# Optimization experiments

Measured on AMD Instinct MI355X. Metric: run time of the kernel, lower is better.

Reference implementation:

```python
import jax, jax.numpy as jnp
import numpy as np

B, H, W = 1, 32, 32
C, G, K = 128, 4, 15
GC = C // G          # group channels = 32
K2 = K * K           # 225
RED = 4              # SE reduction
KHID = 32            # kernel_net hidden


def setup_inputs() -> dict:
    key = jax.random.key(0)
    ks = jax.random.split(key, 24)
    def n(k, shape, s=0.02):
        return jax.random.normal(k, shape, jnp.float32) * s
    inp = {
        'x': jax.random.normal(ks[0], (B, H, W, C), jnp.float32),
        # scalars (torch: raw_sigma init = softplus^{-1}(0.3), base_offset_scale = 0.1)
        'raw_sigma': jnp.asarray(float(np.log(np.expm1(0.3))), jnp.float32),
        'base_offset_scale': jnp.asarray(0.1, jnp.float32),
        # input/output projections
        'w_in': n(ks[1], (C, C)), 'b_in': jnp.zeros((C,), jnp.float32),
        'w_out': n(ks[2], (C, C)), 'b_out': jnp.zeros((C,), jnp.float32),
        # dw_conv: depthwise 3x3 (HWIO, I=1 per group) + pointwise 1x1
        'dw_k': n(ks[3], (3, 3, 1, C), 0.1), 'dw_b': jnp.zeros((C,), jnp.float32),
        'pw_w': n(ks[4], (C, C)), 'pw_b': jnp.zeros((C,), jnp.float32),
        # offset / mask nets (zero-init in torch; small random here to exercise gather)
        'off_w': n(ks[5], (C, G * K2 * 2), 0.01), 'off_b': n(ks[6], (G * K2 * 2,), 0.01),
        'msk_w': n(ks[7], (C, G * K2), 0.01), 'msk_b': n(ks[8], (G * K2,), 0.01),
        # kernel_net: 2 -> 32 -> 32 -> G*GC
        'k1_w': n(ks[9], (2, KHID), 0.3), 'k1_b': jnp.zeros((KHID,), jnp.float32),
        'k2_w': n(ks[10], (KHID, KHID), 0.2), 'k2_b': jnp.zeros((KHID,), jnp.float32),
        'k3_w': n(ks[11], (KHID, G * GC), 0.2), 'k3_b': jnp.zeros((G * GC,), jnp.float32),
        # SE block
        'se1_w': n(ks[12], (C, C // RED), 0.1), 'se1_b': jnp.zeros((C // RED,), jnp.float32),
        'se2_w': n(ks[13], (C // RED, C), 0.1), 'se2_b': jnp.zeros((C,), jnp.float32),
    }
    return inp


def reference(x, raw_sigma, base_offset_scale, w_in, b_in, w_out, b_out,
              dw_k, dw_b, pw_w, pw_b, off_w, off_b, msk_w, msk_b,
              k1_w, k1_b, k2_w, k2_b, k3_w, k3_b, se1_w, se1_b, se2_w, se2_b):
    # sigma (scalar path, biases=None)
    sigma = jnp.clip(jax.nn.softplus(raw_sigma), 0.001, 0.5)
    grid = jnp.linspace(-0.5, 0.5, K)

    x_proj = x @ w_in + b_in                                   # [B,H,W,C]

    # dw_conv: depthwise 3x3 -> SiLU -> 1x1
    y = jax.lax.conv_general_dilated(
        x, dw_k, (1, 1), 'SAME',
        dimension_numbers=('NHWC', 'HWIO', 'NHWC'),
        feature_group_count=C) + dw_b
    x_dw = jax.nn.silu(y) @ pw_w + pw_b                        # [B,H,W,C]

    # Gaussian envelope over kernel grid, normalized (scalar sigma -> shape [K,K])
    gh = grid[:, None]; gw = grid[None, :]
    env = jnp.exp(-(gh ** 2 + gw ** 2) / (2.0 * sigma ** 2))
    env = env / jnp.clip(env.sum(), 1e-8)                      # [K,K]

    # dynamic kernel weights from grid positions (*2); replicate torch's
    # contiguous view (K,K,G,gc) -> (G,K2,gc)
    pos = jnp.stack(jnp.meshgrid(grid, grid, indexing='ij'), -1).reshape(K2, 2) * 2.0
    h1 = jax.nn.silu(pos @ k1_w + k1_b)
    h2 = jax.nn.silu(h1 @ k2_w + k2_b)
    kw = (h2 @ k3_w + k3_b).reshape(K, K, G, GC).reshape(G, K2, GC)  # [G,K2,gc]

    offsets = (x_dw @ off_w + off_b).reshape(B, H, W, G, K2, 2) * base_offset_scale
    raw_mask = (x_dw @ msk_w + msk_b).reshape(B, H, W, G, K2) * env.reshape(1, 1, 1, 1, K2)
    attn = jnp.nan_to_num(jax.nn.softmax(raw_mask, axis=-1))   # [B,H,W,G,K2]

    # reference sampling grid (integer offsets -K//2..K//2)
    ref = jnp.linspace(-(K // 2), K // 2, K)
    ref_grid = jnp.stack(jnp.meshgrid(ref, ref, indexing='ij'), -1).reshape(K2, 2)
    pos_h = jnp.arange(H, dtype=jnp.float32).reshape(1, H, 1, 1, 1)
    pos_w = jnp.arange(W, dtype=jnp.float32).reshape(1, 1, W, 1, 1)

    abs_h = pos_h + ref_grid[:, 0].reshape(1, 1, 1, 1, K2) + offsets[..., 0]
    abs_w = pos_w + ref_grid[:, 1].reshape(1, 1, 1, 1, K2) + offsets[..., 1]
    ah = jnp.clip(abs_h, 0.0, H - 1); aw = jnp.clip(abs_w, 0.0, W - 1)
    hf = jnp.clip(ah.astype(jnp.int32), 0, H - 1)
    wf = jnp.clip(aw.astype(jnp.int32), 0, W - 1)
    hc = jnp.clip(hf + 1, 0, H - 1)
    wc = jnp.clip(wf + 1, 0, W - 1)
    hw = ah - hf.astype(jnp.float32)
    ww = aw - wf.astype(jnp.float32)
    valid = (~((abs_h < 0) | (abs_h > H - 1) | (abs_w < 0) | (abs_w > W - 1))).astype(jnp.float32)

    x_g = x_proj.reshape(B, H, W, G, GC)
    b_idx = jnp.arange(B).reshape(B, 1, 1, 1, 1)
    g_idx = jnp.arange(G).reshape(1, 1, 1, G, 1)
    def gather(hi, wi):
        return x_g[b_idx, hi, wi, g_idx]                       # [B,H,W,G,K2,gc]

    sampled = (gather(hf, wf) * ((1 - hw) * (1 - ww) * valid)[..., None]
             + gather(hf, wc) * ((1 - hw) * ww * valid)[..., None]
             + gather(hc, wf) * (hw * (1 - ww) * valid)[..., None]
             + gather(hc, wc) * (hw * ww * valid)[..., None])

    sampled = sampled * kw.reshape(1, 1, 1, G, K2, GC)
    out = jnp.einsum('bhwgkc,bhwgk->bhwgc', sampled, attn).reshape(B, H, W, C)

    # SE block (mask=None, bias=None)
    pooled = out.mean(axis=(1, 2), keepdims=True)
    scale = jax.nn.sigmoid(jax.nn.silu(pooled @ se1_w + se1_b) @ se2_w + se2_b)
    out = out * scale

    return out @ w_out + b_out
```

## Files before the change

### kernel.cpp

```cpp
#include <hip/hip_runtime.h>
#include <math.h>

constexpr int H = 32, W = 32, C = 128, G = 4, K = 15, K2 = 225, GC = 32;
constexpr int NPIX = H * W;
constexpr int NOFF = G * K2 * 2;
constexpr int NMSK = G * K2;
constexpr int NTOT = NOFF + NMSK;
constexpr int KHID = 32;

constexpr size_t WS_ENV    = 0;
constexpr size_t WS_KW     = 256;
constexpr size_t WS_SCALE  = 29184;
constexpr size_t WS_PART   = 29312;
constexpr size_t WS_XPROJ  = 33792;
constexpr size_t WS_XDW    = 164864;
constexpr size_t WS_OUTPRE = 295936;
constexpr size_t WS_OFFS   = 427008;
constexpr size_t WS_MASK   = 2270208;

__device__ __forceinline__ float sigmoidf_(float v) { return 1.f / (1.f + expf(-v)); }
__device__ __forceinline__ float siluf_(float v)    { return v / (1.f + expf(-v)); }

__device__ __forceinline__ void mlp_point(int k2i, int lane,
                                          const float* __restrict__ k1_w, const float* __restrict__ k1_b,
                                          const float* __restrict__ k2_w, const float* __restrict__ k2_b,
                                          const float* __restrict__ k3_w, const float* __restrict__ k3_b,
                                          float* __restrict__ ws) {
    int i = k2i / 15, j = k2i % 15;
    float ph = (-0.5f + (float)i * (1.f / 14.f)) * 2.f;
    float pw = (-0.5f + (float)j * (1.f / 14.f)) * 2.f;
    float h1[KHID], h2[KHID];
#pragma unroll
    for (int m = 0; m < KHID; m++)
        h1[m] = siluf_(fmaf(ph, k1_w[m], fmaf(pw, k1_w[KHID + m], k1_b[m])));
#pragma unroll
    for (int m = 0; m < KHID; m++) {
        float a = k2_b[m];
#pragma unroll
        for (int q = 0; q < KHID; q++) a = fmaf(h1[q], k2_w[q * KHID + m], a);
        h2[m] = siluf_(a);
    }
#pragma unroll
    for (int t = 0; t < 2; t++) {
        int col = lane + t * 64;
        float a = k3_b[col];
#pragma unroll
        for (int q = 0; q < KHID; q++) a = fmaf(h2[q], k3_w[q * C + col], a);
        ws[WS_KW + (size_t)k2i * C + col] = a;
    }
}

__global__ __launch_bounds__(256) void prep_kernel(const float* __restrict__ raw_sigma,
                             const float* __restrict__ k1_w, const float* __restrict__ k1_b,
                             const float* __restrict__ k2_w, const float* __restrict__ k2_b,
                             const float* __restrict__ k3_w, const float* __restrict__ k3_b,
                             float* __restrict__ ws) {
    int tid = threadIdx.x;
    if (blockIdx.x == 0) {
        __shared__ float red[256];
        float xs = raw_sigma[0];
        float sp = fmaxf(xs, 0.f) + log1pf(expf(-fabsf(xs)));
        float sigma = fminf(fmaxf(sp, 0.001f), 0.5f);
        float inv2s2 = 1.f / (2.f * sigma * sigma);
        int i = tid / 15, j = tid % 15;
        float e = 0.f;
        if (tid < K2) {
            float gi = -0.5f + (float)i * (1.f / 14.f);
            float gj = -0.5f + (float)j * (1.f / 14.f);
            e = expf(-(gi * gi + gj * gj) * inv2s2);
        }
        red[tid] = e;
        __syncthreads();
        for (int s = 128; s > 0; s >>= 1) {
            if (tid < s) red[tid] += red[tid + s];
            __syncthreads();
        }
        float esum = fmaxf(red[0], 1e-8f);
        if (tid < K2) ws[WS_ENV + tid] = e / esum;
        if (tid < 64) mlp_point(224, tid, k1_w, k1_b, k2_w, k2_b, k3_w, k3_b, ws);
    } else {
        int k2i = (blockIdx.x - 1) * 4 + (tid >> 6);
        mlp_point(k2i, tid & 63, k1_w, k1_b, k2_w, k2_b, k3_w, k3_b, ws);
    }
}

__global__ __launch_bounds__(256) void front_kernel(const float* __restrict__ x,
                             const float* __restrict__ w_in, const float* __restrict__ b_in,
                             const float* __restrict__ dw_k, const float* __restrict__ dw_b,
                             const float* __restrict__ pw_w, const float* __restrict__ pw_b,
                             float* __restrict__ ws) {
    int p0 = blockIdx.x * 4;
    int tid = threadIdx.x;
    int c = tid & 127;
    int pp = tid >> 7;
    __shared__ float xs[4][C], ts[4][C];
#pragma unroll
    for (int q = 0; q < 2; q++) {
        int px = pp * 2 + q;
        int p = p0 + px;
        int h = p >> 5, w = p & 31;
        xs[px][c] = x[(size_t)p * C + c];
        float y = dw_b[c];
#pragma unroll
        for (int dy = 0; dy < 3; dy++) {
            int hh = h + dy - 1;
            if (hh < 0 || hh >= H) continue;
#pragma unroll
            for (int dx = 0; dx < 3; dx++) {
                int wq = w + dx - 1;
                if (wq < 0 || wq >= W) continue;
                y = fmaf(x[((size_t)hh * W + wq) * C + c], dw_k[(dy * 3 + dx) * C + c], y);
            }
        }
        ts[px][c] = siluf_(y);
    }
    __syncthreads();
    float ap0 = b_in[c], ap1 = b_in[c], ad0 = pw_b[c], ad1 = pw_b[c];
    int b0 = pp * 2, b1 = pp * 2 + 1;
    for (int i = 0; i < C; i += 4) {
#pragma unroll
        for (int u = 0; u < 4; u++) {
            float wi = w_in[(size_t)(i + u) * C + c];
            float pi = pw_w[(size_t)(i + u) * C + c];
            ap0 = fmaf(xs[b0][i + u], wi, ap0);
            ap1 = fmaf(xs[b1][i + u], wi, ap1);
            ad0 = fmaf(ts[b0][i + u], pi, ad0);
            ad1 = fmaf(ts[b1][i + u], pi, ad1);
        }
    }
    ws[WS_XPROJ + (size_t)(p0 + b0) * C + c] = ap0;
    ws[WS_XPROJ + (size_t)(p0 + b1) * C + c] = ap1;
    ws[WS_XDW  + (size_t)(p0 + b0) * C + c] = ad0;
    ws[WS_XDW  + (size_t)(p0 + b1) * C + c] = ad1;
}

__global__ __launch_bounds__(256) void offmsk_gemm(const float* __restrict__ A,
                                                   const float* __restrict__ off_w,
                                                   const float* __restrict__ off_b,
                                                   const float* __restrict__ msk_w,
                                                   const float* __restrict__ msk_b,
                                                   const float* __restrict__ bos,
                                                   const float* __restrict__ env,
                                                   float* __restrict__ offs_out,
                                                   float* __restrict__ mask_out) {
    __shared__ float At[32][72];
    __shared__ float Bs[32][64];
    int tid = threadIdx.x;
    int c0 = blockIdx.x * 64;
    int p0 = blockIdx.y * 64;
    int tx = tid & 15, ty = tid >> 4;

    float acc[4][4];
#pragma unroll
    for (int i = 0; i < 4; i++)
#pragma unroll
        for (int j = 0; j < 4; j++) acc[i][j] = 0.f;

    int cL = (tid * 4) & 63;
    int kL = (tid * 4) >> 6;
    int cB = c0 + cL;
    const float* bptr = nullptr; int bstride = 0;
    if (cB < NOFF)       { bptr = off_w + cB;          bstride = NOFF; }
    else if (cB < NTOT)  { bptr = msk_w + (cB - NOFF); bstride = NMSK; }
    int rA = tid >> 3, k4A = (tid & 7) * 4;

    for (int kt = 0; kt < C; kt += 32) {
        if (kt) __syncthreads();
#pragma unroll
        for (int pass = 0; pass < 2; pass++) {
            int r = rA + pass * 32;
            float4 v = *(const float4*)&A[(size_t)(p0 + r) * C + kt + k4A];
            At[k4A + 0][r] = v.x; At[k4A + 1][r] = v.y;
            At[k4A + 2][r] = v.z; At[k4A + 3][r] = v.w;
            int k = kL + pass * 16;
            float4 bv = make_float4(0.f, 0.f, 0.f, 0.f);
            if (bptr) bv = *(const float4*)&bptr[(size_t)(kt + k) * bstride];
            *(float4*)&Bs[k][cL] = bv;
        }
        __syncthreads();
#pragma unroll
        for (int k = 0; k < 32; k++) {
            float4 a4 = *(const float4*)&At[k][ty * 4];
            float4 b4 = *(const float4*)&Bs[k][tx * 4];
            const float av[4] = {a4.x, a4.y, a4.z, a4.w};
            const float bv[4] = {b4.x, b4.y, b4.z, b4.w};
#pragma unroll
            for (int i = 0; i < 4; i++)
#pragma unroll
                for (int j = 0; j < 4; j++)
                    acc[i][j] = fmaf(av[i], bv[j], acc[i][j]);
        }
    }

    int colbase = c0 + tx * 4;
    if (colbase >= NTOT) return;
    float bias[4], sc[4];
    float* obase;
    int ostride;
    if (colbase < NOFF) {
        float s = bos[0];
#pragma unroll
        for (int j = 0; j < 4; j++) { bias[j] = off_b[colbase + j]; sc[j] = s; }
        obase = offs_out + colbase; ostride = NOFF;
    } else {
        int m0 = colbase - NOFF;
#pragma unroll
        for (int j = 0; j < 4; j++) { bias[j] = msk_b[m0 + j]; sc[j] = env[(m0 + j) % K2]; }
        obase = mask_out + m0; ostride = NMSK;
    }
#pragma unroll
    for (int i = 0; i < 4; i++) {
        size_t row = (size_t)(p0 + ty * 4 + i);
        float4 r0 = make_float4((acc[i][0] + bias[0]) * sc[0], (acc[i][1] + bias[1]) * sc[1],
                                (acc[i][2] + bias[2]) * sc[2], (acc[i][3] + bias[3]) * sc[3]);
        *(float4*)&obase[row * ostride] = r0;
    }
}

__global__ __launch_bounds__(256) void sampler_kernel(const float* __restrict__ ws_offs,
                                                      const float* __restrict__ ws_mask,
                                                      const float* __restrict__ xproj,
                                                      const float* __restrict__ kwf,
                                                      float* __restrict__ outpre) {
    int p0 = blockIdx.x * 2;
    int h = p0 >> 5;
    int tid = threadIdx.x;

    __shared__ float   attn_s[2][NMSK];
    __shared__ float4  wgt_s[2][NMSK];
    __shared__ ushort4 loc_s[2][NMSK];

    {
        int half = tid >> 5;
        int l32 = tid & 31;
        int px = half >> 2, g = half & 3;
        const float* mrow = ws_mask + (size_t)(p0 + px) * NMSK + g * K2;
        float v[8];
        float mx = -1e30f;
#pragma unroll
        for (int q = 0; q < 8; q++) {
            int k = l32 + q * 32;
            v[q] = (k < K2) ? mrow[k] : -1e30f;
            mx = fmaxf(mx, v[q]);
        }
#pragma unroll
        for (int s = 16; s > 0; s >>= 1) mx = fmaxf(mx, __shfl_xor(mx, s));
        float sum = 0.f;
#pragma unroll
        for (int q = 0; q < 8; q++) {
            int k = l32 + q * 32;
            v[q] = (k < K2) ? expf(v[q] - mx) : 0.f;
            sum += v[q];
        }
#pragma unroll
        for (int s = 16; s > 0; s >>= 1) sum += __shfl_xor(sum, s);
        float inv = 1.f / sum;
#pragma unroll
        for (int q = 0; q < 8; q++) {
            int k = l32 + q * 32;
            if (k < K2) attn_s[px][g * K2 + k] = v[q] * inv;
        }
    }
    __syncthreads();

    for (int e = tid; e < 2 * NMSK; e += 256) {
        int px = (e >= NMSK) ? 1 : 0;
        int m = e - px * NMSK;
        int g = m / K2;
        int k = m - g * K2;
        int p = p0 + px;
        int w = p & 31;
        float2 o = *(const float2*)&ws_offs[(size_t)p * NOFF + m * 2];
        float abs_h = (float)(h + k / 15 - 7) + o.x;
        float abs_w = (float)(w + k % 15 - 7) + o.y;
        float validf = (abs_h < 0.f || abs_h > 31.f || abs_w < 0.f || abs_w > 31.f) ? 0.f : 1.f;
        float ah = fminf(fmaxf(abs_h, 0.f), 31.f);
        float aw = fminf(fmaxf(abs_w, 0.f), 31.f);
        int hf = (int)ah, wf = (int)aw;
        int hc = min(hf + 1, 31), wc = min(wf + 1, 31);
        float hwt = ah - (float)hf, wwt = aw - (float)wf;
        float a = attn_s[px][m] * validf;
        float u0 = 1.f - hwt, u1 = 1.f - wwt;
        wgt_s[px][m] = make_float4(a * u0 * u1, a * u0 * wwt, a * hwt * u1, a * hwt * wwt);
        loc_s[px][m] = make_ushort4((unsigned short)(hf * W + wf), (unsigned short)(hf * W + wc),
                                    (unsigned short)(hc * W + wf), (unsigned short)(hc * W + wc));
    }
    __syncthreads();

    {
        int cq = tid & 7;
        int s  = (tid >> 3) & 3;
        int g  = (tid >> 5) & 3;
        int px = tid >> 7;
        int k0 = (s * K2) >> 2;
        int k1 = ((s + 1) * K2) >> 2;
        const float* xpg = xproj + g * GC + cq * 4;
        const float* kwg = kwf + (size_t)g * (K2 * GC) + cq * 4;
        float4 acc = make_float4(0.f, 0.f, 0.f, 0.f);
        for (int k = k0; k < k1; k++) {
            int m = g * K2 + k;
            ushort4 L  = loc_s[px][m];
            float4  Wv = wgt_s[px][m];
            float4 x00 = *(const float4*)(xpg + (int)L.x * C);
            float4 x01 = *(const float4*)(xpg + (int)L.y * C);
            float4 x10 = *(const float4*)(xpg + (int)L.z * C);
            float4 x11 = *(const float4*)(xpg + (int)L.w * C);
            float4 kw4 = *(const float4*)(kwg + k * GC);
            float sx = fmaf(Wv.w, x11.x, fmaf(Wv.z, x10.x, fmaf(Wv.y, x01.x, Wv.x * x00.x)));
            float sy = fmaf(Wv.w, x11.y, fmaf(Wv.z, x10.y, fmaf(Wv.y, x01.y, Wv.x * x00.y)));
            float sz = fmaf(Wv.w, x11.z, fmaf(Wv.z, x10.z, fmaf(Wv.y, x01.z, Wv.x * x00.z)));
            float sw = fmaf(Wv.w, x11.w, fmaf(Wv.z, x10.w, fmaf(Wv.y, x01.w, Wv.x * x00.w)));
            acc.x = fmaf(kw4.x, sx, acc.x);
            acc.y = fmaf(kw4.y, sy, acc.y);
            acc.z = fmaf(kw4.z, sz, acc.z);
            acc.w = fmaf(kw4.w, sw, acc.w);
        }
        acc.x += __shfl_xor(acc.x, 8);  acc.y += __shfl_xor(acc.y, 8);
        acc.z += __shfl_xor(acc.z, 8);  acc.w += __shfl_xor(acc.w, 8);
        acc.x += __shfl_xor(acc.x, 16); acc.y += __shfl_xor(acc.y, 16);
        acc.z += __shfl_xor(acc.z, 16); acc.w += __shfl_xor(acc.w, 16);
        if (s == 0)
            *(float4*)&outpre[(size_t)(p0 + px) * C + g * GC + cq * 4] = acc;
    }
}

__global__ void reduce1_kernel(const float* __restrict__ outpre, float* __restrict__ part) {
    int b = blockIdx.x;
    int c = threadIdx.x;
    float s = 0.f;
    for (int q = 0; q < 32; q++) s += outpre[(size_t)(b * 32 + q) * C + c];
    part[(size_t)b * C + c] = s;
}

__global__ void se_kernel(const float* __restrict__ part,
                          const float* __restrict__ se1_w, const float* __restrict__ se1_b,
                          const float* __restrict__ se2_w, const float* __restrict__ se2_b,
                          float* __restrict__ scale_out) {
    __shared__ float pooled[C];
    __shared__ float hid[KHID];
    int tid = threadIdx.x;
    float s = 0.f;
    for (int b = 0; b < 32; b++) s += part[(size_t)b * C + tid];
    pooled[tid] = s * (1.f / 1024.f);
    __syncthreads();
    if (tid < KHID) {
        float a = se1_b[tid];
        for (int cc = 0; cc < C; cc++) a = fmaf(pooled[cc], se1_w[cc * KHID + tid], a);
        hid[tid] = siluf_(a);
    }
    __syncthreads();
    float a = se2_b[tid];
#pragma unroll
    for (int q = 0; q < KHID; q++) a = fmaf(hid[q], se2_w[q * C + tid], a);
    scale_out[tid] = sigmoidf_(a);
}

__global__ __launch_bounds__(256) void final_kernel(const float* __restrict__ outpre,
                             const float* __restrict__ scale,
                             const float* __restrict__ w_out, const float* __restrict__ b_out,
                             float* __restrict__ out) {
    int p0 = blockIdx.x * 4;
    int tid = threadIdx.x;
    int c = tid & 127;
    int pp = tid >> 7;
    __shared__ float v[4][C];
    float scv = scale[c];
#pragma unroll
    for (int q = 0; q < 2; q++) {
        int px = pp * 2 + q;
        v[px][c] = outpre[(size_t)(p0 + px) * C + c] * scv;
    }
    __syncthreads();
    float a0 = b_out[c], a1 = b_out[c];
    int b0 = pp * 2, b1 = pp * 2 + 1;
    for (int i = 0; i < C; i += 4) {
#pragma unroll
        for (int u = 0; u < 4; u++) {
            float wv = w_out[(size_t)(i + u) * C + c];
            a0 = fmaf(v[b0][i + u], wv, a0);
            a1 = fmaf(v[b1][i + u], wv, a1);
        }
    }
    out[(size_t)(p0 + b0) * C + c] = a0;
    out[(size_t)(p0 + b1) * C + c] = a1;
}

extern "C" void kernel_launch(void* const* d_in, const int* in_sizes, int n_in,
                              void* d_out, int out_size, void* d_ws, size_t ws_size,
                              hipStream_t stream) {
    const float* x         = (const float*)d_in[0];
    const float* raw_sigma = (const float*)d_in[1];
    const float* bos       = (const float*)d_in[2];
    const float* w_in      = (const float*)d_in[3];
    const float* b_in      = (const float*)d_in[4];
    const float* w_out     = (const float*)d_in[5];
    const float* b_out     = (const float*)d_in[6];
    const float* dw_k      = (const float*)d_in[7];
    const float* dw_b      = (const float*)d_in[8];
    const float* pw_w      = (const float*)d_in[9];
    const float* pw_b      = (const float*)d_in[10];
    const float* off_w     = (const float*)d_in[11];
    const float* off_b     = (const float*)d_in[12];
    const float* msk_w     = (const float*)d_in[13];
    const float* msk_b     = (const float*)d_in[14];
    const float* k1_w      = (const float*)d_in[15];
    const float* k1_b      = (const float*)d_in[16];
    const float* k2_w      = (const float*)d_in[17];
    const float* k2_b      = (const float*)d_in[18];
    const float* k3_w      = (const float*)d_in[19];
    const float* k3_b      = (const float*)d_in[20];
    const float* se1_w     = (const float*)d_in[21];
    const float* se1_b     = (const float*)d_in[22];
    const float* se2_w     = (const float*)d_in[23];
    const float* se2_b     = (const float*)d_in[24];

    float* ws  = (float*)d_ws;
    float* out = (float*)d_out;

    prep_kernel<<<57, 256, 0, stream>>>(raw_sigma, k1_w, k1_b, k2_w, k2_b, k3_w, k3_b, ws);
    front_kernel<<<NPIX / 4, 256, 0, stream>>>(x, w_in, b_in, dw_k, dw_b, pw_w, pw_b, ws);

    dim3 gg((NTOT + 63) / 64, NPIX / 64);
    offmsk_gemm<<<gg, 256, 0, stream>>>(ws + WS_XDW, off_w, off_b, msk_w, msk_b, bos,
                                        ws + WS_ENV, ws + WS_OFFS, ws + WS_MASK);

    sampler_kernel<<<NPIX / 2, 256, 0, stream>>>(ws + WS_OFFS, ws + WS_MASK, ws + WS_XPROJ,
                                                 ws + WS_KW, ws + WS_OUTPRE);

    reduce1_kernel<<<32, C, 0, stream>>>(ws + WS_OUTPRE, ws + WS_PART);
    se_kernel<<<1, C, 0, stream>>>(ws + WS_PART, se1_w, se1_b, se2_w, se2_b, ws + WS_SCALE);
    final_kernel<<<NPIX / 4, 256, 0, stream>>>(ws + WS_OUTPRE, ws + WS_SCALE, w_out, b_out, out);
}
```

Measured before the change: 81.26 us.

## Fuse prep/front and SE/final kernels, enlarge offset GEMM tiles

Merges the prep and front kernels into one launch and moves the SE pooling partial sums into the sampler epilogue. Every block of a new finale kernel redundantly computes the SE scale before applying the output projection, which cuts the launch count from seven to four and removes the separate reduce and SE passes. The offset/mask GEMM moves from 64x64 tiles with 4x4 per-thread outputs to 128x128 tiles with 8x8, plus tail guards on partial columns. The changes trade launch overhead for redundant SE work in all 256 finale blocks, and the larger GEMM tiles mean fewer blocks and higher register pressure.

```diff
diff --git a/kernel.cpp b/kernel.cpp
--- a/kernel.cpp
+++ b/kernel.cpp
@@ -8,24 +8,23 @@
 constexpr int NTOT = NOFF + NMSK;
 constexpr int KHID = 32;
 
-constexpr size_t WS_ENV    = 0;
-constexpr size_t WS_KW     = 256;
-constexpr size_t WS_SCALE  = 29184;
-constexpr size_t WS_PART   = 29312;
-constexpr size_t WS_XPROJ  = 33792;
-constexpr size_t WS_XDW    = 164864;
-constexpr size_t WS_OUTPRE = 295936;
-constexpr size_t WS_OFFS   = 427008;
-constexpr size_t WS_MASK   = 2270208;
+constexpr size_t WS_ENV    = 128;
+constexpr size_t WS_KW     = 384;
+constexpr size_t WS_PART   = 29184;
+constexpr size_t WS_XPROJ  = 94720;
+constexpr size_t WS_XDW    = 225792;
+constexpr size_t WS_OFFS   = 356864;
+constexpr size_t WS_MASK   = 2200064;
+constexpr size_t WS_OUTPRE = 3121664;
 
 __device__ __forceinline__ float sigmoidf_(float v) { return 1.f / (1.f + expf(-v)); }
 __device__ __forceinline__ float siluf_(float v)    { return v / (1.f + expf(-v)); }
 
 __device__ __forceinline__ void mlp_point(int k2i, int lane,
-                                          const float* __restrict__ k1_w, const float* __restrict__ k1_b,
-                                          const float* __restrict__ k2_w, const float* __restrict__ k2_b,
-                                          const float* __restrict__ k3_w, const float* __restrict__ k3_b,
-                                          float* __restrict__ ws) {
+        const float* __restrict__ k1_w, const float* __restrict__ k1_b,
+        const float* __restrict__ k2_w, const float* __restrict__ k2_b,
+        const float* __restrict__ k3_w, const float* __restrict__ k3_b,
+        float* __restrict__ ws) {
     int i = k2i / 15, j = k2i % 15;
     float ph = (-0.5f + (float)i * (1.f / 14.f)) * 2.f;
     float pw = (-0.5f + (float)j * (1.f / 14.f)) * 2.f;
@@ -50,114 +49,110 @@
     }
 }
 
-__global__ __launch_bounds__(256) void prep_kernel(const float* __restrict__ raw_sigma,
-                             const float* __restrict__ k1_w, const float* __restrict__ k1_b,
-                             const float* __restrict__ k2_w, const float* __restrict__ k2_b,
-                             const float* __restrict__ k3_w, const float* __restrict__ k3_b,
-                             float* __restrict__ ws) {
+__global__ __launch_bounds__(256) void prep_front_kernel(const float* __restrict__ x,
+        const float* __restrict__ raw_sigma,
+        const float* __restrict__ w_in, const float* __restrict__ b_in,
+        const float* __restrict__ dw_k, const float* __restrict__ dw_b,
+        const float* __restrict__ pw_w, const float* __restrict__ pw_b,
+        const float* __restrict__ k1_w, const float* __restrict__ k1_b,
+        const float* __restrict__ k2_w, const float* __restrict__ k2_b,
+        const float* __restrict__ k3_w, const float* __restrict__ k3_b,
+        float* __restrict__ ws) {
     int tid = threadIdx.x;
-    if (blockIdx.x == 0) {
-        __shared__ float red[256];
-        float xs = raw_sigma[0];
-        float sp = fmaxf(xs, 0.f) + log1pf(expf(-fabsf(xs)));
-        float sigma = fminf(fmaxf(sp, 0.001f), 0.5f);
-        float inv2s2 = 1.f / (2.f * sigma * sigma);
-        int i = tid / 15, j = tid % 15;
-        float e = 0.f;
-        if (tid < K2) {
-            float gi = -0.5f + (float)i * (1.f / 14.f);
-            float gj = -0.5f + (float)j * (1.f / 14.f);
-            e = expf(-(gi * gi + gj * gj) * inv2s2);
-        }
-        red[tid] = e;
+    int b = blockIdx.x;
+    if (b < 256) {
+        __shared__ float xs[4][C], ts[4][C];
+        int p0 = b * 4;
+        int c = tid & 127, pp = tid >> 7;
+#pragma unroll
+        for (int q = 0; q < 2; q++) {
+            int px = pp * 2 + q;
+            int p = p0 + px;
+            int h = p >> 5, w = p & 31;
+            xs[px][c] = x[(size_t)p * C + c];
+            float y = dw_b[c];
+#pragma unroll
+            for (int dy = 0; dy < 3; dy++) {
+                int hh = h + dy - 1;
+                if (hh < 0 || hh >= H) continue;
+#pragma unroll
+                for (int dx = 0; dx < 3; dx++) {
+                    int wq = w + dx - 1;
+                    if (wq < 0 || wq >= W) continue;
+                    y = fmaf(x[((size_t)hh * W + wq) * C + c], dw_k[(dy * 3 + dx) * C + c], y);
+                }
+            }
+            ts[px][c] = siluf_(y);
+        }
         __syncthreads();
-        for (int s = 128; s > 0; s >>= 1) {
-            if (tid < s) red[tid] += red[tid + s];
+        float ap0 = b_in[c], ap1 = ap0, ad0 = pw_b[c], ad1 = ad0;
+        int b0 = pp * 2, b1 = pp * 2 + 1;
+        for (int i = 0; i < C; i += 4) {
+#pragma unroll
+            for (int u = 0; u < 4; u++) {
+                float wi = w_in[(size_t)(i + u) * C + c];
+                float pi = pw_w[(size_t)(i + u) * C + c];
+                ap0 = fmaf(xs[b0][i + u], wi, ap0);
+                ap1 = fmaf(xs[b1][i + u], wi, ap1);
+                ad0 = fmaf(ts[b0][i + u], pi, ad0);
+                ad1 = fmaf(ts[b1][i + u], pi, ad1);
+            }
+        }
+        ws[WS_XPROJ + (size_t)(p0 + b0) * C + c] = ap0;
+        ws[WS_XPROJ + (size_t)(p0 + b1) * C + c] = ap1;
+        ws[WS_XDW  + (size_t)(p0 + b0) * C + c] = ad0;
+        ws[WS_XDW  + (size_t)(p0 + b1) * C + c] = ad1;
+    } else {
+        int mb = b - 256;
+        if (mb == 0) {
+            __shared__ float red[256];
+            float xsg = raw_sigma[0];
+            float sp = fmaxf(xsg, 0.f) + log1pf(expf(-fabsf(xsg)));
+            float sigma = fminf(fmaxf(sp, 0.001f), 0.5f);
+            float inv2s2 = 1.f / (2.f * sigma * sigma);
+            int i = tid / 15, j = tid % 15;
+            float e = 0.f;
+            if (tid < K2) {
+                float gi = -0.5f + (float)i * (1.f / 14.f);
+                float gj = -0.5f + (float)j * (1.f / 14.f);
+                e = expf(-(gi * gi + gj * gj) * inv2s2);
+            }
+            red[tid] = e;
             __syncthreads();
-        }
-        float esum = fmaxf(red[0], 1e-8f);
-        if (tid < K2) ws[WS_ENV + tid] = e / esum;
-        if (tid < 64) mlp_point(224, tid, k1_w, k1_b, k2_w, k2_b, k3_w, k3_b, ws);
-    } else {
-        int k2i = (blockIdx.x - 1) * 4 + (tid >> 6);
-        mlp_point(k2i, tid & 63, k1_w, k1_b, k2_w, k2_b, k3_w, k3_b, ws);
-    }
-}
-
-__global__ __launch_bounds__(256) void front_kernel(const float* __restrict__ x,
-                             const float* __restrict__ w_in, const float* __restrict__ b_in,
-                             const float* __restrict__ dw_k, const float* __restrict__ dw_b,
-                             const float* __restrict__ pw_w, const float* __restrict__ pw_b,
-                             float* __restrict__ ws) {
-    int p0 = blockIdx.x * 4;
+            for (int s = 128; s > 0; s >>= 1) {
+                if (tid < s) red[tid] += red[tid + s];
+                __syncthreads();
+            }
+            float esum = fmaxf(red[0], 1e-8f);
+            if (tid < K2) ws[WS_ENV + tid] = e / esum;
+            if (tid < 64) mlp_point(224, tid, k1_w, k1_b, k2_w, k2_b, k3_w, k3_b, ws);
+        } else {
+            int k2i = (mb - 1) * 4 + (tid >> 6);
+            mlp_point(k2i, tid & 63, k1_w, k1_b, k2_w, k2_b, k3_w, k3_b, ws);
+        }
+    }
+}
+
+__global__ __launch_bounds__(256) void offmsk_gemm(const float* __restrict__ A,
+        const float* __restrict__ off_w, const float* __restrict__ off_b,
+        const float* __restrict__ msk_w, const float* __restrict__ msk_b,
+        const float* __restrict__ bos, const float* __restrict__ env,
+        float* __restrict__ offs_out, float* __restrict__ mask_out) {
+    __shared__ float At[32][132];
+    __shared__ float Bs[32][128];
     int tid = threadIdx.x;
-    int c = tid & 127;
-    int pp = tid >> 7;
-    __shared__ float xs[4][C], ts[4][C];
-#pragma unroll
-    for (int q = 0; q < 2; q++) {
-        int px = pp * 2 + q;
-        int p = p0 + px;
-        int h = p >> 5, w = p & 31;
-        xs[px][c] = x[(size_t)p * C + c];
-        float y = dw_b[c];
-#pragma unroll
-        for (int dy = 0; dy < 3; dy++) {
-            int hh = h + dy - 1;
-            if (hh < 0 || hh >= H) continue;
-#pragma unroll
-            for (int dx = 0; dx < 3; dx++) {
-                int wq = w + dx - 1;
-                if (wq < 0 || wq >= W) continue;
-                y = fmaf(x[((size_t)hh * W + wq) * C + c], dw_k[(dy * 3 + dx) * C + c], y);
-            }
-        }
-        ts[px][c] = siluf_(y);
-    }
-    __syncthreads();
-    float ap0 = b_in[c], ap1 = b_in[c], ad0 = pw_b[c], ad1 = pw_b[c];
-    int b0 = pp * 2, b1 = pp * 2 + 1;
-    for (int i = 0; i < C; i += 4) {
-#pragma unroll
-        for (int u = 0; u < 4; u++) {
-            float wi = w_in[(size_t)(i + u) * C + c];
-            float pi = pw_w[(size_t)(i + u) * C + c];
-            ap0 = fmaf(xs[b0][i + u], wi, ap0);
-            ap1 = fmaf(xs[b1][i + u], wi, ap1);
-            ad0 = fmaf(ts[b0][i + u], pi, ad0);
-            ad1 = fmaf(ts[b1][i + u], pi, ad1);
-        }
-    }
-    ws[WS_XPROJ + (size_t)(p0 + b0) * C + c] = ap0;
-    ws[WS_XPROJ + (size_t)(p0 + b1) * C + c] = ap1;
-    ws[WS_XDW  + (size_t)(p0 + b0) * C + c] = ad0;
-    ws[WS_XDW  + (size_t)(p0 + b1) * C + c] = ad1;
-}
-
-__global__ __launch_bounds__(256) void offmsk_gemm(const float* __restrict__ A,
-                                                   const float* __restrict__ off_w,
-                                                   const float* __restrict__ off_b,
-                                                   const float* __restrict__ msk_w,
-                                                   const float* __restrict__ msk_b,
-                                                   const float* __restrict__ bos,
-                                                   const float* __restrict__ env,
-                                                   float* __restrict__ offs_out,
-                                                   float* __restrict__ mask_out) {
-    __shared__ float At[32][72];
-    __shared__ float Bs[32][64];
-    int tid = threadIdx.x;
-    int c0 = blockIdx.x * 64;
-    int p0 = blockIdx.y * 64;
+    int c0 = blockIdx.x * 128;
+    int p0 = blockIdx.y * 128;
     int tx = tid & 15, ty = tid >> 4;
 
-    float acc[4][4];
-#pragma unroll
-    for (int i = 0; i < 4; i++)
-#pragma unroll
-        for (int j = 0; j < 4; j++) acc[i][j] = 0.f;
-
-    int cL = (tid * 4) & 63;
-    int kL = (tid * 4) >> 6;
+    float acc[8][8];
+#pragma unroll
+    for (int i = 0; i < 8; i++)
+#pragma unroll
+        for (int j = 0; j < 8; j++) acc[i][j] = 0.f;
+
+    int cL = (tid & 31) * 4;
+    int kB = tid >> 5;
     int cB = c0 + cL;
     const float* bptr = nullptr; int bstride = 0;
     if (cB < NOFF)       { bptr = off_w + cB;          bstride = NOFF; }
@@ -167,68 +162,88 @@
     for (int kt = 0; kt < C; kt += 32) {
         if (kt) __syncthreads();
 #pragma unroll
-        for (int pass = 0; pass < 2; pass++) {
+        for (int pass = 0; pass < 4; pass++) {
             int r = rA + pass * 32;
             float4 v = *(const float4*)&A[(size_t)(p0 + r) * C + kt + k4A];
             At[k4A + 0][r] = v.x; At[k4A + 1][r] = v.y;
             At[k4A + 2][r] = v.z; At[k4A + 3][r] = v.w;
-            int k = kL + pass * 16;
+        }
+#pragma unroll
+        for (int pass = 0; pass < 4; pass++) {
+            int k = kB + pass * 8;
             float4 bv = make_float4(0.f, 0.f, 0.f, 0.f);
             if (bptr) bv = *(const float4*)&bptr[(size_t)(kt + k) * bstride];
             *(float4*)&Bs[k][cL] = bv;
         }
         __syncthreads();
-#pragma unroll
+#pragma unroll 4
         for (int k = 0; k < 32; k++) {
-            float4 a4 = *(const float4*)&At[k][ty * 4];
-            float4 b4 = *(const float4*)&Bs[k][tx * 4];
-            const float av[4] = {a4.x, a4.y, a4.z, a4.w};
-            const float bv[4] = {b4.x, b4.y, b4.z, b4.w};
-#pragma unroll
-            for (int i = 0; i < 4; i++)
-#pragma unroll
-                for (int j = 0; j < 4; j++)
+            float4 a0 = *(const float4*)&At[k][ty * 8];
+            float4 a1 = *(const float4*)&At[k][ty * 8 + 4];
+            float4 b0 = *(const float4*)&Bs[k][tx * 8];
+            float4 b1 = *(const float4*)&Bs[k][tx * 8 + 4];
+            const float av[8] = {a0.x, a0.y, a0.z, a0.w, a1.x, a1.y, a1.z, a1.w};
+            const float bv[8] = {b0.x, b0.y, b0.z, b0.w, b1.x, b1.y, b1.z, b1.w};
+#pragma unroll
+            for (int i = 0; i < 8; i++)
+#pragma unroll
+                for (int j = 0; j < 8; j++)
                     acc[i][j] = fmaf(av[i], bv[j], acc[i][j]);
         }
     }
 
-    int colbase = c0 + tx * 4;
+    int colbase = c0 + tx * 8;
     if (colbase >= NTOT) return;
-    float bias[4], sc[4];
+    bool full = (colbase + 8) <= NTOT;
+    float bias[8], sc[8];
     float* obase;
     int ostride;
     if (colbase < NOFF) {
         float s = bos[0];
 #pragma unroll
-        for (int j = 0; j < 4; j++) { bias[j] = off_b[colbase + j]; sc[j] = s; }
+        for (int j = 0; j < 8; j++) { bias[j] = off_b[colbase + j]; sc[j] = s; }
         obase = offs_out + colbase; ostride = NOFF;
     } else {
         int m0 = colbase - NOFF;
 #pragma unroll
-        for (int j = 0; j < 4; j++) { bias[j] = msk_b[m0 + j]; sc[j] = env[(m0 + j) % K2]; }
+        for (int j = 0; j < 8; j++) {
+            if (colbase + j < NTOT) { bias[j] = msk_b[m0 + j]; sc[j] = env[(m0 + j) % K2]; }
+            else                    { bias[j] = 0.f; sc[j] = 0.f; }
+        }
         obase = mask_out + m0; ostride = NMSK;
     }
 #pragma unroll
-    for (int i = 0; i < 4; i++) {
-        size_t row = (size_t)(p0 + ty * 4 + i);
-        float4 r0 = make_float4((acc[i][0] + bias[0]) * sc[0], (acc[i][1] + bias[1]) * sc[1],
-                                (acc[i][2] + bias[2]) * sc[2], (acc[i][3] + bias[3]) * sc[3]);
-        *(float4*)&obase[row * ostride] = r0;
+    for (int i = 0; i < 8; i++) {
+        size_t row = (size_t)(p0 + ty * 8 + i);
+        if (full) {
+            float4 r0 = make_float4((acc[i][0] + bias[0]) * sc[0], (acc[i][1] + bias[1]) * sc[1],
+                                    (acc[i][2] + bias[2]) * sc[2], (acc[i][3] + bias[3]) * sc[3]);
+            float4 r1 = make_float4((acc[i][4] + bias[4]) * sc[4], (acc[i][5] + bias[5]) * sc[5],
+                                    (acc[i][6] + bias[6]) * sc[6], (acc[i][7] + bias[7]) * sc[7]);
+            *(float4*)&obase[row * ostride]     = r0;
+            *(float4*)&obase[row * ostride + 4] = r1;
+        } else {
+#pragma unroll
+            for (int j = 0; j < 8; j++)
+                if (colbase + j < NTOT)
+                    obase[row * ostride + j] = (acc[i][j] + bias[j]) * sc[j];
+        }
     }
 }
 
 __global__ __launch_bounds__(256) void sampler_kernel(const float* __restrict__ ws_offs,
-                                                      const float* __restrict__ ws_mask,
-                                                      const float* __restrict__ xproj,
-                                                      const float* __restrict__ kwf,
-                                                      float* __restrict__ outpre) {
-    int p0 = blockIdx.x * 2;
+        const float* __restrict__ ws_mask, const float* __restrict__ xproj,
+        const float* __restrict__ kwf, float* __restrict__ outpre,
+        float* __restrict__ partial) {
+    int blk = blockIdx.x;
+    int p0 = blk * 2;
     int h = p0 >> 5;
     int tid = threadIdx.x;
 
     __shared__ float   attn_s[2][NMSK];
     __shared__ float4  wgt_s[2][NMSK];
     __shared__ ushort4 loc_s[2][NMSK];
+    __shared__ float   outp[2][C];
 
     {
         int half = tid >> 5;
@@ -297,6 +312,7 @@
         const float* xpg = xproj + g * GC + cq * 4;
         const float* kwg = kwf + (size_t)g * (K2 * GC) + cq * 4;
         float4 acc = make_float4(0.f, 0.f, 0.f, 0.f);
+#pragma unroll 2
         for (int k = k0; k < k1; k++) {
             int m = g * K2 + k;
             ushort4 L  = loc_s[px][m];
@@ -319,29 +335,45 @@
         acc.z += __shfl_xor(acc.z, 8);  acc.w += __shfl_xor(acc.w, 8);
         acc.x += __shfl_xor(acc.x, 16); acc.y += __shfl_xor(acc.y, 16);
         acc.z += __shfl_xor(acc.z, 16); acc.w += __shfl_xor(acc.w, 16);
-        if (s == 0)
+        if (s == 0) {
+            *(float4*)&outp[px][g * GC + cq * 4] = acc;
             *(float4*)&outpre[(size_t)(p0 + px) * C + g * GC + cq * 4] = acc;
-    }
-}
-
-__global__ void reduce1_kernel(const float* __restrict__ outpre, float* __restrict__ part) {
-    int b = blockIdx.x;
-    int c = threadIdx.x;
-    float s = 0.f;
-    for (int q = 0; q < 32; q++) s += outpre[(size_t)(b * 32 + q) * C + c];
-    part[(size_t)b * C + c] = s;
-}
-
-__global__ void se_kernel(const float* __restrict__ part,
-                          const float* __restrict__ se1_w, const float* __restrict__ se1_b,
-                          const float* __restrict__ se2_w, const float* __restrict__ se2_b,
-                          float* __restrict__ scale_out) {
+        }
+    }
+    __syncthreads();
+    if (tid < C)
+        partial[(size_t)blk * C + tid] = outp[0][tid] + outp[1][tid];
+}
+
+__global__ __launch_bounds__(256) void finale_kernel(const float* __restrict__ outpre,
+        const float* __restrict__ partial,
+        const float* __restrict__ se1_w, const float* __restrict__ se1_b,
+        const float* __restrict__ se2_w, const float* __restrict__ se2_b,
+        const float* __restrict__ w_out, const float* __restrict__ b_out,
+        float* __restrict__ out) {
+    int tid = threadIdx.x;
+    __shared__ float tmp[8][132];
     __shared__ float pooled[C];
     __shared__ float hid[KHID];
-    int tid = threadIdx.x;
-    float s = 0.f;
-    for (int b = 0; b < 32; b++) s += part[(size_t)b * C + tid];
-    pooled[tid] = s * (1.f / 1024.f);
+    __shared__ float scl[C];
+    __shared__ float v[4][C];
+
+    {
+        int bg = tid >> 5, c4 = (tid & 31) * 4;
+        float4 s4 = make_float4(0.f, 0.f, 0.f, 0.f);
+        for (int i = 0; i < 64; i++) {
+            float4 pv = *(const float4*)&partial[(size_t)(bg * 64 + i) * C + c4];
+            s4.x += pv.x; s4.y += pv.y; s4.z += pv.z; s4.w += pv.w;
+        }
+        *(float4*)&tmp[bg][c4] = s4;
+    }
+    __syncthreads();
+    if (tid < C) {
+        float s = 0.f;
+#pragma unroll
+        for (int g = 0; g < 8; g++) s += tmp[g][tid];
+        pooled[tid] = s * (1.f / 1024.f);
+    }
     __syncthreads();
     if (tid < KHID) {
         float a = se1_b[tid];
@@ -349,26 +381,20 @@
         hid[tid] = siluf_(a);
     }
     __syncthreads();
-    float a = se2_b[tid];
-#pragma unroll
-    for (int q = 0; q < KHID; q++) a = fmaf(hid[q], se2_w[q * C + tid], a);
-    scale_out[tid] = sigmoidf_(a);
-}
-
-__global__ __launch_bounds__(256) void final_kernel(const float* __restrict__ outpre,
-                             const float* __restrict__ scale,
-                             const float* __restrict__ w_out, const float* __restrict__ b_out,
-                             float* __restrict__ out) {
+    if (tid < C) {
+        float a = se2_b[tid];
+#pragma unroll
+        for (int q = 0; q < KHID; q++) a = fmaf(hid[q], se2_w[q * C + tid], a);
+        scl[tid] = sigmoidf_(a);
+    }
+    __syncthreads();
+
     int p0 = blockIdx.x * 4;
-    int tid = threadIdx.x;
-    int c = tid & 127;
-    int pp = tid >> 7;
-    __shared__ float v[4][C];
-    float scv = scale[c];
+    int c = tid & 127, pp = tid >> 7;
 #pragma unroll
     for (int q = 0; q < 2; q++) {
         int px = pp * 2 + q;
-        v[px][c] = outpre[(size_t)(p0 + px) * C + c] * scv;
+        v[px][c] = outpre[(size_t)(p0 + px) * C + c] * scl[c];
     }
     __syncthreads();
     float a0 = b_out[c], a1 = b_out[c];
@@ -417,17 +443,18 @@
     float* ws  = (float*)d_ws;
     float* out = (float*)d_out;
 
-    prep_kernel<<<57, 256, 0, stream>>>(raw_sigma, k1_w, k1_b, k2_w, k2_b, k3_w, k3_b, ws);
-    front_kernel<<<NPIX / 4, 256, 0, stream>>>(x, w_in, b_in, dw_k, dw_b, pw_w, pw_b, ws);
-
-    dim3 gg((NTOT + 63) / 64, NPIX / 64);
+    prep_front_kernel<<<313, 256, 0, stream>>>(x, raw_sigma, w_in, b_in, dw_k, dw_b,
+                                               pw_w, pw_b, k1_w, k1_b, k2_w, k2_b,
+                                               k3_w, k3_b, ws);
+
+    dim3 gg((NTOT + 127) / 128, NPIX / 128);
     offmsk_gemm<<<gg, 256, 0, stream>>>(ws + WS_XDW, off_w, off_b, msk_w, msk_b, bos,
                                         ws + WS_ENV, ws + WS_OFFS, ws + WS_MASK);
 
     sampler_kernel<<<NPIX / 2, 256, 0, stream>>>(ws + WS_OFFS, ws + WS_MASK, ws + WS_XPROJ,
-                                                 ws + WS_KW, ws + WS_OUTPRE);
-
-    reduce1_kernel<<<32, C, 0, stream>>>(ws + WS_OUTPRE, ws + WS_PART);
-    se_kernel<<<1, C, 0, stream>>>(ws + WS_PART, se1_w, se1_b, se2_w, se2_b, ws + WS_SCALE);
-    final_kernel<<<NPIX / 4, 256, 0, stream>>>(ws + WS_OUTPRE, ws + WS_SCALE, w_out, b_out, out);
-}
+                                                 ws + WS_KW, ws + WS_OUTPRE, ws + WS_PART);
+
+    finale_kernel<<<NPIX / 4, 256, 0, stream>>>(ws + WS_OUTPRE, ws + WS_PART,
+                                                se1_w, se1_b, se2_w, se2_b,
+                                                w_out, b_out, out);
+}
```

New measurement: 79.63 us. 1.02x faster.
